# Optimization experiments

Measured on AMD Instinct MI355X. Metric: run time of the kernel, lower is better.

## Reference

```python
import jax, jax.numpy as jnp
import numpy as np


def setup_inputs() -> dict:
    key = jax.random.key(0)
    k1, k2, k3, k4 = jax.random.split(key, 4)
    B, S, d_in, d_out = 4, 2048, 1024, 1024
    x = jax.random.normal(k1, (B, S, d_in), dtype=jnp.float32)
    # weights stored as [d_in, d_out] (transpose of torch Linear weight), scaled like default init
    scale = 1.0 / np.sqrt(d_in)
    Wq = jax.random.normal(k2, (d_in, d_out), dtype=jnp.float32) * scale
    Wk = jax.random.normal(k3, (d_in, d_out), dtype=jnp.float32) * scale
    Wv = jax.random.normal(k4, (d_in, d_out), dtype=jnp.float32) * scale
    return {"x": x, "Wq": Wq, "Wk": Wk, "Wv": Wv}


def reference(x, Wq, Wk, Wv):
    # x: [B, S, d_in]; projections: [B, S, d_out]
    q = jnp.einsum("bsd,de->bse", x, Wq)
    k = jnp.einsum("bsd,de->bse", x, Wk)
    v = jnp.einsum("bsd,de->bse", x, Wv)
    d_out = k.shape[-1]
    # full S x S scores (naive, as in original)
    scores = jnp.einsum("bqe,bke->bqk", q, k)
    # NOTE: original applies softmax over ALL keys first, then multiplies by
    # a lower-triangular causal mask WITHOUT renormalizing. Reproduce exactly.
    weights = jax.nn.softmax(scores / jnp.sqrt(jnp.float32(d_out)), axis=-1)
    S = scores.shape[1]
    mask = jnp.tril(jnp.ones((S, S), dtype=weights.dtype))
    masked = weights * mask  # [B, S, S]
    context = jnp.einsum("bqk,bke->bqe", masked, v)
    return context
```

## Files before the change

kernel.cpp:

```cpp
#include <hip/hip_runtime.h>
#include <hip/hip_bf16.h>
#include <hip/hip_fp16.h>

typedef __attribute__((ext_vector_type(8))) short bf16x8;
typedef __attribute__((ext_vector_type(4))) float f32x4;

__device__ __forceinline__ unsigned short f2bf(float f) {
    unsigned u = __float_as_uint(f);
    u += 0x7fffu + ((u >> 16) & 1u);
    return (unsigned short)(u >> 16);
}

#define GLOAD_LDS16(g, l)                                                           \
    __builtin_amdgcn_global_load_lds(                                               \
        (const __attribute__((address_space(1))) void*)(g),                         \
        (__attribute__((address_space(3))) void*)(l), 16, 0, 0)

#define TBM 256
#define TBN 256
#define TBK 64

template <int OMODE>
__global__ __launch_bounds__(512, 2) void gemm256(
    const unsigned short* __restrict__ A, const unsigned short* __restrict__ B,
    void* __restrict__ Cv, int M, int N, int K,
    long long sA, long long sB, long long sC) {
    __shared__ unsigned short lds[2][4][128 * 64];

    const int bz = blockIdx.z;
    A += (size_t)bz * (size_t)sA;
    B += (size_t)bz * (size_t)sB;

    const int bm = blockIdx.x, bn = blockIdx.y;
    const int tid = threadIdx.x;
    const int wid = tid >> 6, lane = tid & 63;
    const int wr = wid >> 2, wc = wid & 3;
    const int frow = lane & 15, kgrp = lane >> 4;
    const int nt = K / TBK;

    const unsigned short* Abase = A + (size_t)(bm * TBM) * K;
    const unsigned short* Bbase = B + (size_t)(bn * TBN) * K;

    auto STAGE_H = [&](const unsigned short* gtb, int kt, unsigned short* dsthalf) {
#pragma unroll
        for (int ld = 0; ld < 2; ++ld) {
            const int c = tid + ld * 512;
            const int row = c >> 3, c8 = c & 7;
            GLOAD_LDS16(gtb + (size_t)row * K + kt * TBK + ((c8 ^ (row & 7)) << 3),
                        (char*)dsthalf + ld * 8192 + wid * 1024);
        }
    };

    f32x4 acc[8][4];
#pragma unroll
    for (int i = 0; i < 8; ++i)
#pragma unroll
        for (int j = 0; j < 4; ++j) acc[i][j] = (f32x4){0.f, 0.f, 0.f, 0.f};

    STAGE_H(Bbase, 0, &lds[0][2][0]);
    STAGE_H(Bbase + 128 * (size_t)K, 0, &lds[0][3][0]);
    STAGE_H(Abase, 0, &lds[0][0][0]);
    STAGE_H(Abase + 128 * (size_t)K, 0, &lds[0][1][0]);

    for (int t = 0; t < nt; ++t) {
        const int buf = t & 1, bufN = buf ^ 1;
        const unsigned short* Ah = &lds[buf][wr][0];
        const unsigned short* Bh = &lds[buf][2 + (wc >> 1)][0];

        if (t + 1 < nt) {
            STAGE_H(Bbase, t + 1, &lds[bufN][2][0]);
            STAGE_H(Bbase + 128 * (size_t)K, t + 1, &lds[bufN][3][0]);
            asm volatile("s_waitcnt vmcnt(4)" ::: "memory");
        } else {
            asm volatile("s_waitcnt vmcnt(0)" ::: "memory");
        }
        __builtin_amdgcn_s_barrier();

        bf16x8 bfrag[4][2];
#pragma unroll
        for (int n = 0; n < 4; ++n) {
            const int rB = (wc & 1) * 64 + n * 16 + frow;
            const int sw = (rB & 7) << 3;
#pragma unroll
            for (int kk = 0; kk < 2; ++kk)
                bfrag[n][kk] =
                    *(const bf16x8*)&Bh[rB * 64 + ((((kk << 2) + kgrp) << 3) ^ sw)];
        }
        {
            bf16x8 afrag[2][2];
#pragma unroll
            for (int m2 = 0; m2 < 2; ++m2) {
                const int rA = m2 * 16 + frow;
                const int sw = (rA & 7) << 3;
#pragma unroll
                for (int kk = 0; kk < 2; ++kk)
                    afrag[m2][kk] =
                        *(const bf16x8*)&Ah[rA * 64 + ((((kk << 2) + kgrp) << 3) ^ sw)];
            }
            __builtin_amdgcn_s_setprio(1);
#pragma unroll
            for (int m2 = 0; m2 < 2; ++m2)
#pragma unroll
                for (int n = 0; n < 4; ++n)
#pragma unroll
                    for (int kk = 0; kk < 2; ++kk)
                        acc[m2][n] = __builtin_amdgcn_mfma_f32_16x16x32_bf16(
                            afrag[m2][kk], bfrag[n][kk], acc[m2][n], 0, 0, 0);
            __builtin_amdgcn_s_setprio(0);
        }

#pragma unroll
        for (int q = 1; q < 4; ++q) {
            if (q == 1 && t + 1 < nt) STAGE_H(Abase, t + 1, &lds[bufN][0][0]);
            if (q == 2 && t + 1 < nt)
                STAGE_H(Abase + 128 * (size_t)K, t + 1, &lds[bufN][1][0]);
            bf16x8 afrag[2][2];
#pragma unroll
            for (int m2 = 0; m2 < 2; ++m2) {
                const int rA = q * 32 + m2 * 16 + frow;
                const int sw = (rA & 7) << 3;
#pragma unroll
                for (int kk = 0; kk < 2; ++kk)
                    afrag[m2][kk] =
                        *(const bf16x8*)&Ah[rA * 64 + ((((kk << 2) + kgrp) << 3) ^ sw)];
            }
            __builtin_amdgcn_s_setprio(1);
#pragma unroll
            for (int m2 = 0; m2 < 2; ++m2)
#pragma unroll
                for (int n = 0; n < 4; ++n)
#pragma unroll
                    for (int kk = 0; kk < 2; ++kk)
                        acc[q * 2 + m2][n] = __builtin_amdgcn_mfma_f32_16x16x32_bf16(
                            afrag[m2][kk], bfrag[n][kk], acc[q * 2 + m2][n], 0, 0, 0);
            __builtin_amdgcn_s_setprio(0);
        }
    }

    const size_t row0 = (size_t)bm * TBM + wr * 128 + kgrp * 4;
    const int col0 = bn * TBN + wc * 64 + frow;
    if (OMODE == 0) {
        unsigned short* Cp = (unsigned short*)Cv + (size_t)bz * (size_t)sC;
#pragma unroll
        for (int mi = 0; mi < 8; ++mi)
#pragma unroll
            for (int rr = 0; rr < 4; ++rr) {
                unsigned short* op = Cp + (row0 + mi * 16 + rr) * N + col0;
#pragma unroll
                for (int n = 0; n < 4; ++n) op[n * 16] = f2bf(acc[mi][n][rr]);
            }
    } else {
        unsigned short* Cp = (unsigned short*)Cv + (size_t)bz * (size_t)sC;
#pragma unroll
        for (int mi = 0; mi < 8; ++mi)
#pragma unroll
            for (int rr = 0; rr < 4; ++rr) {
                unsigned short* op = Cp + (row0 + mi * 16 + rr) * N + col0;
#pragma unroll
                for (int n = 0; n < 4; ++n)
                    op[n * 16] =
                        __half_as_ushort(__float2half(acc[mi][n][rr] * 0.03125f));
            }
    }
}

#define BM 128
#define BN 128
#define BK 32

__global__ __launch_bounds__(256) void gemm_bt_f32(
    const unsigned short* __restrict__ A, const unsigned short* __restrict__ B,
    float* __restrict__ C, int M, int N, int K,
    long long sA, long long sB, long long sC, int causal) {
    __shared__ unsigned short As[2][BM * BK];
    __shared__ unsigned short Bs[2][BN * BK];

    const int bz = blockIdx.z;
    A += (size_t)bz * (size_t)sA;
    B += (size_t)bz * (size_t)sB;

    const int bm = blockIdx.x, bn = blockIdx.y;
    const int tid = threadIdx.x;
    const int wid = tid >> 6;
    const int lane = tid & 63;
    const int wr = wid >> 1, wc = wid & 1;
    const int frow = lane & 15;
    const int kgrp = lane >> 4;

    int nt = K / BK;
    if (causal) {
        int lim = (bm + 1) * (BM / BK);
        if (lim < nt) nt = lim;
    }

    const int c0 = (wid * 2 + 0) * 64 + lane;
    const int c1 = (wid * 2 + 1) * 64 + lane;
    const unsigned short* Abase = A + (size_t)(bm * BM) * K;
    const unsigned short* Bbase = B + (size_t)(bn * BN) * K;

    auto STAGE = [&](int kt, int buf) {
        const unsigned short* Ag = Abase + kt * BK;
        const unsigned short* Bg = Bbase + kt * BK;
        GLOAD_LDS16(Ag + (size_t)(c0 >> 2) * K + (c0 & 3) * 8,
                    (char*)&As[buf][0] + (wid * 2 + 0) * 1024);
        GLOAD_LDS16(Bg + (size_t)(c0 >> 2) * K + (c0 & 3) * 8,
                    (char*)&Bs[buf][0] + (wid * 2 + 0) * 1024);
        GLOAD_LDS16(Ag + (size_t)(c1 >> 2) * K + (c1 & 3) * 8,
                    (char*)&As[buf][0] + (wid * 2 + 1) * 1024);
        GLOAD_LDS16(Bg + (size_t)(c1 >> 2) * K + (c1 & 3) * 8,
                    (char*)&Bs[buf][0] + (wid * 2 + 1) * 1024);
    };

    f32x4 acc[4][4];
#pragma unroll
    for (int mi = 0; mi < 4; ++mi)
#pragma unroll
        for (int ni = 0; ni < 4; ++ni) acc[mi][ni] = (f32x4){0.f, 0.f, 0.f, 0.f};

    STAGE(0, 0);
    __syncthreads();

    for (int kt = 0; kt < nt; ++kt) {
        const int buf = kt & 1;
        if (kt + 1 < nt) STAGE(kt + 1, buf ^ 1);
        bf16x8 af[4], bfr[4];
#pragma unroll
        for (int mi = 0; mi < 4; ++mi) {
            int row = wr * 64 + mi * 16 + frow;
            af[mi] = *(const bf16x8*)&As[buf][row * BK + kgrp * 8];
        }
#pragma unroll
        for (int ni = 0; ni < 4; ++ni) {
            int col = wc * 64 + ni * 16 + frow;
            bfr[ni] = *(const bf16x8*)&Bs[buf][col * BK + kgrp * 8];
        }
#pragma unroll
        for (int mi = 0; mi < 4; ++mi)
#pragma unroll
            for (int ni = 0; ni < 4; ++ni)
                acc[mi][ni] = __builtin_amdgcn_mfma_f32_16x16x32_bf16(
                    af[mi], bfr[ni], acc[mi][ni], 0, 0, 0);
        __syncthreads();
    }

    const size_t row0 = (size_t)bm * BM + wr * 64 + kgrp * 4;
    const int col0 = bn * BN + wc * 64 + frow;
    float* Cp = C + (size_t)bz * (size_t)sC;
#pragma unroll
    for (int mi = 0; mi < 4; ++mi)
#pragma unroll
        for (int r = 0; r < 4; ++r) {
            float* op = Cp + (row0 + mi * 16 + r) * N + col0;
#pragma unroll
            for (int ni = 0; ni < 4; ++ni) op[ni * 16] = acc[mi][ni][r];
        }
}

__global__ __launch_bounds__(256) void cvt_f32_bf16(
    const float* __restrict__ in, unsigned short* __restrict__ out, int n) {
    int idx = blockIdx.x * blockDim.x + threadIdx.x;
    int stride = gridDim.x * blockDim.x;
    for (int i = idx * 4; i < n; i += stride * 4) {
        float4 v = *(const float4*)(in + i);
        ushort4 o;
        o.x = f2bf(v.x); o.y = f2bf(v.y); o.z = f2bf(v.z); o.w = f2bf(v.w);
        *(ushort4*)(out + i) = o;
    }
}

__global__ __launch_bounds__(256) void transpose_cvt_w(
    const float* __restrict__ in, unsigned short* __restrict__ out, int Kd, int Nd) {
    __shared__ float t[32][33];
    const int bz = blockIdx.z;
    in += (size_t)bz * Kd * Nd;
    out += (size_t)bz * Kd * Nd;
    const int tr = blockIdx.y * 32, tc = blockIdx.x * 32;
    const int r = threadIdx.x >> 3, c4 = (threadIdx.x & 7) * 4;
    float4 v = *(const float4*)&in[(size_t)(tr + r) * Nd + tc + c4];
    t[r][c4 + 0] = v.x; t[r][c4 + 1] = v.y; t[r][c4 + 2] = v.z; t[r][c4 + 3] = v.w;
    __syncthreads();
    ushort4 o;
    o.x = f2bf(t[c4 + 0][r]); o.y = f2bf(t[c4 + 1][r]);
    o.z = f2bf(t[c4 + 2][r]); o.w = f2bf(t[c4 + 3][r]);
    *(ushort4*)&out[(size_t)(tc + r) * Kd + tr + c4] = o;
}

__global__ __launch_bounds__(256) void transpose_bf16(
    const unsigned short* __restrict__ in, unsigned short* __restrict__ out,
    int R, int Cc) {
    __shared__ unsigned short t[32][36];
    const int bz = blockIdx.z;
    in += (size_t)bz * R * Cc;
    out += (size_t)bz * R * Cc;
    const int tr = blockIdx.y * 32, tc = blockIdx.x * 32;
    const int r = threadIdx.x >> 3, c4 = (threadIdx.x & 7) * 4;
    ushort4 v = *(const ushort4*)&in[(size_t)(tr + r) * Cc + tc + c4];
    t[r][c4 + 0] = v.x; t[r][c4 + 1] = v.y; t[r][c4 + 2] = v.z; t[r][c4 + 3] = v.w;
    __syncthreads();
    ushort4 o;
    o.x = t[c4 + 0][r]; o.y = t[c4 + 1][r]; o.z = t[c4 + 2][r]; o.w = t[c4 + 3][r];
    *(ushort4*)&out[(size_t)(tc + r) * R + tr + c4] = o;
}

__global__ __launch_bounds__(256) void softmax_mask(unsigned short* S, int Sd) {
    const int i = blockIdx.x;
    const int b = blockIdx.y;
    unsigned short* row = S + ((size_t)b * Sd + (size_t)i) * Sd;
    const int t = threadIdx.x;
    const int lane = t & 63, wid = t >> 6;

    ushort4 h0 = *(const ushort4*)(row + t * 8);
    ushort4 h1 = *(const ushort4*)(row + t * 8 + 4);
    float v[8];
    v[0] = __half2float(__ushort_as_half(h0.x));
    v[1] = __half2float(__ushort_as_half(h0.y));
    v[2] = __half2float(__ushort_as_half(h0.z));
    v[3] = __half2float(__ushort_as_half(h0.w));
    v[4] = __half2float(__ushort_as_half(h1.x));
    v[5] = __half2float(__ushort_as_half(h1.y));
    v[6] = __half2float(__ushort_as_half(h1.z));
    v[7] = __half2float(__ushort_as_half(h1.w));

    float m = v[0];
#pragma unroll
    for (int j = 1; j < 8; ++j) m = fmaxf(m, v[j]);
#pragma unroll
    for (int o = 32; o; o >>= 1) m = fmaxf(m, __shfl_xor(m, o));
    __shared__ float redm[4];
    __shared__ float reds[4];
    if (lane == 0) redm[wid] = m;
    __syncthreads();
    m = fmaxf(fmaxf(redm[0], redm[1]), fmaxf(redm[2], redm[3]));

    float e[8], s = 0.f;
#pragma unroll
    for (int j = 0; j < 8; ++j) {
        e[j] = __expf(v[j] - m);
        s += e[j];
    }
#pragma unroll
    for (int o = 32; o; o >>= 1) s += __shfl_xor(s, o);
    if (lane == 0) reds[wid] = s;
    __syncthreads();
    s = reds[0] + reds[1] + reds[2] + reds[3];
    const float rinv = 1.0f / s;

    const int base = t * 8;
    ushort4 o0, o1;
    o0.x = (base + 0 <= i) ? f2bf(e[0] * rinv) : 0;
    o0.y = (base + 1 <= i) ? f2bf(e[1] * rinv) : 0;
    o0.z = (base + 2 <= i) ? f2bf(e[2] * rinv) : 0;
    o0.w = (base + 3 <= i) ? f2bf(e[3] * rinv) : 0;
    o1.x = (base + 4 <= i) ? f2bf(e[4] * rinv) : 0;
    o1.y = (base + 5 <= i) ? f2bf(e[5] * rinv) : 0;
    o1.z = (base + 6 <= i) ? f2bf(e[6] * rinv) : 0;
    o1.w = (base + 7 <= i) ? f2bf(e[7] * rinv) : 0;
    *(ushort4*)(row + t * 8) = o0;
    *(ushort4*)(row + t * 8 + 4) = o1;
}

extern "C" void kernel_launch(void* const* d_in, const int* in_sizes, int n_in,
                              void* d_out, int out_size, void* d_ws, size_t ws_size,
                              hipStream_t stream) {
    const int B = 4, S = 2048, D = 1024;
    const size_t M = (size_t)B * S;

    const float* x = (const float*)d_in[0];
    const float* Wq = (const float*)d_in[1];
    float* out = (float*)d_out;

    unsigned short* xb = (unsigned short*)d_ws;
    unsigned short* Wt = xb + M * D;
    unsigned short* Qb = Wt + 3 * (size_t)D * D;
    unsigned short* Kb = Qb + M * D;
    unsigned short* Vb = Kb + M * D;
    unsigned short* Vt = Vb + M * D;
    unsigned short* Sc = Vt + M * D;
    const size_t need =
        (size_t)(M * D * 5 + 3 * (size_t)D * D + (size_t)B * S * S) * 2;
    if (ws_size < need) return;

    cvt_f32_bf16<<<2048, 256, 0, stream>>>(x, xb, (int)(M * D));
    dim3 tg(D / 32, D / 32, 1);
    transpose_cvt_w<<<tg, 256, 0, stream>>>((const float*)d_in[1], Wt + 0 * (size_t)D * D, D, D);
    transpose_cvt_w<<<tg, 256, 0, stream>>>((const float*)d_in[2], Wt + 1 * (size_t)D * D, D, D);
    transpose_cvt_w<<<tg, 256, 0, stream>>>((const float*)d_in[3], Wt + 2 * (size_t)D * D, D, D);
    (void)Wq;

    gemm256<0><<<dim3(M / TBM, D / TBN, 3), 512, 0, stream>>>(
        xb, Wt, (void*)Qb, (int)M, D, D, 0LL, (long long)D * D, (long long)(M * D));

    transpose_bf16<<<dim3(D / 32, S / 32, B), 256, 0, stream>>>(Vb, Vt, S, D);

    gemm256<2><<<dim3(S / TBM, S / TBN, B), 512, 0, stream>>>(
        Qb, Kb, (void*)Sc, S, S, D, (long long)S * D, (long long)S * D,
        (long long)S * S);

    softmax_mask<<<dim3(S, B), 256, 0, stream>>>(Sc, S);

    gemm_bt_f32<<<dim3(S / BM, D / BN, B), 256, 0, stream>>>(
        Sc, Vt, out, S, D, S, (long long)S * S, (long long)D * S,
        (long long)S * D, 1);
}
```

Measured before the change: 181.7 us.

## Restructure gemm256 pipeline with deeper B prefetch, XCD remap, causal reverse order

```diff
diff --git a/kernel.cpp b/kernel.cpp
--- a/kernel.cpp
+++ b/kernel.cpp
@@ -31,7 +31,11 @@
     A += (size_t)bz * (size_t)sA;
     B += (size_t)bz * (size_t)sB;
 
-    const int bm = blockIdx.x, bn = blockIdx.y;
+    const int nwg = gridDim.x * gridDim.y;
+    const int old = blockIdx.y * gridDim.x + blockIdx.x;
+    const int nid = (old & 7) * (nwg >> 3) + (old >> 3);
+    const int bm = nid / gridDim.y, bn = nid % gridDim.y;
+
     const int tid = threadIdx.x;
     const int wid = tid >> 6, lane = tid & 63;
     const int wr = wid >> 2, wc = wid & 3;
@@ -57,63 +61,38 @@
 #pragma unroll
         for (int j = 0; j < 4; ++j) acc[i][j] = (f32x4){0.f, 0.f, 0.f, 0.f};
 
+    STAGE_H(Abase, 0, &lds[0][0][0]);
+    STAGE_H(Abase + 128 * (size_t)K, 0, &lds[0][1][0]);
     STAGE_H(Bbase, 0, &lds[0][2][0]);
     STAGE_H(Bbase + 128 * (size_t)K, 0, &lds[0][3][0]);
-    STAGE_H(Abase, 0, &lds[0][0][0]);
-    STAGE_H(Abase + 128 * (size_t)K, 0, &lds[0][1][0]);
+    if (1 < nt) {
+        STAGE_H(Bbase, 1, &lds[1][2][0]);
+        STAGE_H(Bbase + 128 * (size_t)K, 1, &lds[1][3][0]);
+        asm volatile("s_waitcnt vmcnt(4)" ::: "memory");
+    } else {
+        asm volatile("s_waitcnt vmcnt(0)" ::: "memory");
+    }
+    __builtin_amdgcn_s_barrier();
 
     for (int t = 0; t < nt; ++t) {
-        const int buf = t & 1, bufN = buf ^ 1;
+        const int buf = t & 1;
         const unsigned short* Ah = &lds[buf][wr][0];
         const unsigned short* Bh = &lds[buf][2 + (wc >> 1)][0];
-
-        if (t + 1 < nt) {
-            STAGE_H(Bbase, t + 1, &lds[bufN][2][0]);
-            STAGE_H(Bbase + 128 * (size_t)K, t + 1, &lds[bufN][3][0]);
-            asm volatile("s_waitcnt vmcnt(4)" ::: "memory");
-        } else {
-            asm volatile("s_waitcnt vmcnt(0)" ::: "memory");
-        }
-        __builtin_amdgcn_s_barrier();
-
         bf16x8 bfrag[4][2];
-#pragma unroll
-        for (int n = 0; n < 4; ++n) {
-            const int rB = (wc & 1) * 64 + n * 16 + frow;
-            const int sw = (rB & 7) << 3;
-#pragma unroll
-            for (int kk = 0; kk < 2; ++kk)
-                bfrag[n][kk] =
-                    *(const bf16x8*)&Bh[rB * 64 + ((((kk << 2) + kgrp) << 3) ^ sw)];
-        }
-        {
-            bf16x8 afrag[2][2];
-#pragma unroll
-            for (int m2 = 0; m2 < 2; ++m2) {
-                const int rA = m2 * 16 + frow;
-                const int sw = (rA & 7) << 3;
-#pragma unroll
-                for (int kk = 0; kk < 2; ++kk)
-                    afrag[m2][kk] =
-                        *(const bf16x8*)&Ah[rA * 64 + ((((kk << 2) + kgrp) << 3) ^ sw)];
+
+#pragma unroll
+        for (int q = 0; q < 4; ++q) {
+            if (q == 0) {
+#pragma unroll
+                for (int n = 0; n < 4; ++n) {
+                    const int rB = (wc & 1) * 64 + n * 16 + frow;
+                    const int sw = (rB & 7) << 3;
+#pragma unroll
+                    for (int kk = 0; kk < 2; ++kk)
+                        bfrag[n][kk] = *(const bf16x8*)
+                            &Bh[rB * 64 + ((((kk << 2) + kgrp) << 3) ^ sw)];
+                }
             }
-            __builtin_amdgcn_s_setprio(1);
-#pragma unroll
-            for (int m2 = 0; m2 < 2; ++m2)
-#pragma unroll
-                for (int n = 0; n < 4; ++n)
-#pragma unroll
-                    for (int kk = 0; kk < 2; ++kk)
-                        acc[m2][n] = __builtin_amdgcn_mfma_f32_16x16x32_bf16(
-                            afrag[m2][kk], bfrag[n][kk], acc[m2][n], 0, 0, 0);
-            __builtin_amdgcn_s_setprio(0);
-        }
-
-#pragma unroll
-        for (int q = 1; q < 4; ++q) {
-            if (q == 1 && t + 1 < nt) STAGE_H(Abase, t + 1, &lds[bufN][0][0]);
-            if (q == 2 && t + 1 < nt)
-                STAGE_H(Abase + 128 * (size_t)K, t + 1, &lds[bufN][1][0]);
             bf16x8 afrag[2][2];
 #pragma unroll
             for (int m2 = 0; m2 < 2; ++m2) {
@@ -121,9 +100,21 @@
                 const int sw = (rA & 7) << 3;
 #pragma unroll
                 for (int kk = 0; kk < 2; ++kk)
-                    afrag[m2][kk] =
-                        *(const bf16x8*)&Ah[rA * 64 + ((((kk << 2) + kgrp) << 3) ^ sw)];
+                    afrag[m2][kk] = *(const bf16x8*)
+                        &Ah[rA * 64 + ((((kk << 2) + kgrp) << 3) ^ sw)];
             }
+
+            if (q == 0 && t + 1 < nt) STAGE_H(Abase, t + 1, &lds[buf ^ 1][0][0]);
+            if (q == 1 && t + 1 < nt)
+                STAGE_H(Abase + 128 * (size_t)K, t + 1, &lds[buf ^ 1][1][0]);
+            if (q == 2 && t + 2 < nt) STAGE_H(Bbase, t + 2, &lds[buf][2][0]);
+            if (q == 3 && t + 2 < nt)
+                STAGE_H(Bbase + 128 * (size_t)K, t + 2, &lds[buf][3][0]);
+
+            __builtin_amdgcn_s_barrier();
+            asm volatile("s_waitcnt lgkmcnt(0)" ::: "memory");
+            __builtin_amdgcn_sched_barrier(0);
+
             __builtin_amdgcn_s_setprio(1);
 #pragma unroll
             for (int m2 = 0; m2 < 2; ++m2)
@@ -134,6 +125,15 @@
                         acc[q * 2 + m2][n] = __builtin_amdgcn_mfma_f32_16x16x32_bf16(
                             afrag[m2][kk], bfrag[n][kk], acc[q * 2 + m2][n], 0, 0, 0);
             __builtin_amdgcn_s_setprio(0);
+
+            if (q == 3) {
+                if (t + 2 < nt) {
+                    asm volatile("s_waitcnt vmcnt(4)" ::: "memory");
+                } else {
+                    asm volatile("s_waitcnt vmcnt(0)" ::: "memory");
+                }
+            }
+            __builtin_amdgcn_s_barrier();
         }
     }
 
@@ -179,7 +179,9 @@
     A += (size_t)bz * (size_t)sA;
     B += (size_t)bz * (size_t)sB;
 
-    const int bm = blockIdx.x, bn = blockIdx.y;
+    int bmi = blockIdx.x;
+    if (causal) bmi = gridDim.x - 1 - bmi;
+    const int bm = bmi, bn = blockIdx.y;
     const int tid = threadIdx.x;
     const int wid = tid >> 6;
     const int lane = tid & 63;
@@ -271,9 +273,6 @@
 __global__ __launch_bounds__(256) void transpose_cvt_w(
     const float* __restrict__ in, unsigned short* __restrict__ out, int Kd, int Nd) {
     __shared__ float t[32][33];
-    const int bz = blockIdx.z;
-    in += (size_t)bz * Kd * Nd;
-    out += (size_t)bz * Kd * Nd;
     const int tr = blockIdx.y * 32, tc = blockIdx.x * 32;
     const int r = threadIdx.x >> 3, c4 = (threadIdx.x & 7) * 4;
     float4 v = *(const float4*)&in[(size_t)(tr + r) * Nd + tc + c4];
@@ -366,7 +365,6 @@
     const size_t M = (size_t)B * S;
 
     const float* x = (const float*)d_in[0];
-    const float* Wq = (const float*)d_in[1];
     float* out = (float*)d_out;
 
     unsigned short* xb = (unsigned short*)d_ws;
@@ -385,7 +383,6 @@
     transpose_cvt_w<<<tg, 256, 0, stream>>>((const float*)d_in[1], Wt + 0 * (size_t)D * D, D, D);
     transpose_cvt_w<<<tg, 256, 0, stream>>>((const float*)d_in[2], Wt + 1 * (size_t)D * D, D, D);
     transpose_cvt_w<<<tg, 256, 0, stream>>>((const float*)d_in[3], Wt + 2 * (size_t)D * D, D, D);
-    (void)Wq;
 
     gemm256<0><<<dim3(M / TBM, D / TBN, 3), 512, 0, stream>>>(
         xb, Wt, (void*)Qb, (int)M, D, D, 0LL, (long long)D * D, (long long)(M * D));
```

Measured after the change: 190.2 us. 1.05x slower.

## Fuse softmax into QK epilogue row sums and PV operand load

Applied to the files above, without the earlier changes.

```diff
diff --git a/kernel.cpp b/kernel.cpp
--- a/kernel.cpp
+++ b/kernel.cpp
@@ -3,6 +3,7 @@
 #include <hip/hip_fp16.h>
 
 typedef __attribute__((ext_vector_type(8))) short bf16x8;
+typedef __attribute__((ext_vector_type(8))) unsigned short u16x8;
 typedef __attribute__((ext_vector_type(4))) float f32x4;
 
 __device__ __forceinline__ unsigned short f2bf(float f) {
@@ -23,7 +24,7 @@
 template <int OMODE>
 __global__ __launch_bounds__(512, 2) void gemm256(
     const unsigned short* __restrict__ A, const unsigned short* __restrict__ B,
-    void* __restrict__ Cv, int M, int N, int K,
+    void* __restrict__ Cv, float* __restrict__ Zb, int M, int N, int K,
     long long sA, long long sB, long long sC) {
     __shared__ unsigned short lds[2][4][128 * 64];
 
@@ -151,65 +152,106 @@
             }
     } else {
         unsigned short* Cp = (unsigned short*)Cv + (size_t)bz * (size_t)sC;
+        float rs[8][4];
 #pragma unroll
         for (int mi = 0; mi < 8; ++mi)
 #pragma unroll
             for (int rr = 0; rr < 4; ++rr) {
                 unsigned short* op = Cp + (row0 + mi * 16 + rr) * N + col0;
-#pragma unroll
-                for (int n = 0; n < 4; ++n)
-                    op[n * 16] =
-                        __half_as_ushort(__float2half(acc[mi][n][rr] * 0.03125f));
-            }
+                float p = 0.f;
+#pragma unroll
+                for (int n = 0; n < 4; ++n) {
+                    __half h = __float2half(acc[mi][n][rr] * 0.03125f);
+                    op[n * 16] = __half_as_ushort(h);
+                    p += __expf(__half2float(h));
+                }
+                rs[mi][rr] = p;
+            }
+#pragma unroll
+        for (int mi = 0; mi < 8; ++mi)
+#pragma unroll
+            for (int rr = 0; rr < 4; ++rr) {
+                float v = rs[mi][rr];
+                v += __shfl_xor(v, 1);
+                v += __shfl_xor(v, 2);
+                v += __shfl_xor(v, 4);
+                v += __shfl_xor(v, 8);
+                rs[mi][rr] = v;
+            }
+        if (frow == 0) {
+            float* Zr = Zb + (size_t)bz * M + row0;
+#pragma unroll
+            for (int mi = 0; mi < 8; ++mi)
+#pragma unroll
+                for (int rr = 0; rr < 4; ++rr)
+                    atomicAdd(&Zr[mi * 16 + rr], rs[mi][rr]);
+        }
     }
 }
 
-#define BM 128
-#define BN 128
-#define BK 32
-
-__global__ __launch_bounds__(256) void gemm_bt_f32(
-    const unsigned short* __restrict__ A, const unsigned short* __restrict__ B,
-    float* __restrict__ C, int M, int N, int K,
-    long long sA, long long sB, long long sC, int causal) {
-    __shared__ unsigned short As[2][BM * BK];
-    __shared__ unsigned short Bs[2][BN * BK];
+#define PBM 128
+#define PBN 128
+#define PBK 32
+
+__global__ __launch_bounds__(256) void pv_fused(
+    const unsigned short* __restrict__ Sh, const unsigned short* __restrict__ Vt,
+    float* __restrict__ C, const float* __restrict__ Z, int Sd, int Dd) {
+    __shared__ unsigned short As[2][PBM * PBK];
+    __shared__ unsigned short Bs[2][PBN * PBK];
+    __shared__ float rinv_s[PBM];
 
     const int bz = blockIdx.z;
-    A += (size_t)bz * (size_t)sA;
-    B += (size_t)bz * (size_t)sB;
-
-    const int bm = blockIdx.x, bn = blockIdx.y;
+    const int bm = gridDim.x - 1 - blockIdx.x;
+    const int bn = blockIdx.y;
     const int tid = threadIdx.x;
-    const int wid = tid >> 6;
-    const int lane = tid & 63;
+    const int wid = tid >> 6, lane = tid & 63;
     const int wr = wid >> 1, wc = wid & 1;
-    const int frow = lane & 15;
-    const int kgrp = lane >> 4;
-
-    int nt = K / BK;
-    if (causal) {
-        int lim = (bm + 1) * (BM / BK);
-        if (lim < nt) nt = lim;
-    }
-
-    const int c0 = (wid * 2 + 0) * 64 + lane;
-    const int c1 = (wid * 2 + 1) * 64 + lane;
-    const unsigned short* Abase = A + (size_t)(bm * BM) * K;
-    const unsigned short* Bbase = B + (size_t)(bn * BN) * K;
-
-    auto STAGE = [&](int kt, int buf) {
-        const unsigned short* Ag = Abase + kt * BK;
-        const unsigned short* Bg = Bbase + kt * BK;
-        GLOAD_LDS16(Ag + (size_t)(c0 >> 2) * K + (c0 & 3) * 8,
-                    (char*)&As[buf][0] + (wid * 2 + 0) * 1024);
-        GLOAD_LDS16(Bg + (size_t)(c0 >> 2) * K + (c0 & 3) * 8,
-                    (char*)&Bs[buf][0] + (wid * 2 + 0) * 1024);
-        GLOAD_LDS16(Ag + (size_t)(c1 >> 2) * K + (c1 & 3) * 8,
-                    (char*)&As[buf][0] + (wid * 2 + 1) * 1024);
-        GLOAD_LDS16(Bg + (size_t)(c1 >> 2) * K + (c1 & 3) * 8,
-                    (char*)&Bs[buf][0] + (wid * 2 + 1) * 1024);
+    const int frow = lane & 15, kgrp = lane >> 4;
+
+    const unsigned short* Sb =
+        Sh + (size_t)bz * Sd * Sd + (size_t)(bm * PBM) * Sd;
+    const unsigned short* Vb =
+        Vt + (size_t)bz * (size_t)Dd * Sd + (size_t)(bn * PBN) * Sd;
+
+    const int nt = (bm + 1) * (PBM / PBK);
+
+    if (tid < PBM) rinv_s[tid] = 1.0f / Z[(size_t)bz * Sd + bm * PBM + tid];
+
+    auto LOAD_A = [&](int kt, u16x8* areg) {
+#pragma unroll
+        for (int ld = 0; ld < 2; ++ld) {
+            const int c = tid + ld * 256;
+            areg[ld] = *(const u16x8*)(Sb + (size_t)(c >> 2) * Sd + kt * PBK +
+                                       (c & 3) * 8);
+        }
     };
+    auto STAGE_B = [&](int kt, int buf) {
+#pragma unroll
+        for (int ld = 0; ld < 2; ++ld) {
+            const int c = tid + ld * 256;
+            GLOAD_LDS16(Vb + (size_t)(c >> 2) * Sd + kt * PBK + (c & 3) * 8,
+                        (char*)&Bs[buf][0] + (wid * 64 + ld * 256) * 16);
+        }
+    };
+    auto XFORM_WRITE = [&](int kt, int buf, const u16x8* areg) {
+#pragma unroll
+        for (int ld = 0; ld < 2; ++ld) {
+            const int c = tid + ld * 256;
+            const int row = c >> 2;
+            const int rowg = bm * PBM + row;
+            const int colg0 = kt * PBK + (c & 3) * 8;
+            const float ri = rinv_s[row];
+            bf16x8 o;
+#pragma unroll
+            for (int j = 0; j < 8; ++j) {
+                float e = __expf(__half2float(__ushort_as_half(
+                              (unsigned short)areg[ld][j]))) *
+                          ri;
+                o[j] = (colg0 + j <= rowg) ? (short)f2bf(e) : (short)0;
+            }
+            *(bf16x8*)((char*)&As[buf][0] + c * 16) = o;
+        }
+    };
 
     f32x4 acc[4][4];
 #pragma unroll
@@ -217,22 +259,30 @@
 #pragma unroll
         for (int ni = 0; ni < 4; ++ni) acc[mi][ni] = (f32x4){0.f, 0.f, 0.f, 0.f};
 
-    STAGE(0, 0);
+    u16x8 areg[2];
+    LOAD_A(0, areg);
+    STAGE_B(0, 0);
     __syncthreads();
-
-    for (int kt = 0; kt < nt; ++kt) {
-        const int buf = kt & 1;
-        if (kt + 1 < nt) STAGE(kt + 1, buf ^ 1);
+    XFORM_WRITE(0, 0, areg);
+    __syncthreads();
+
+    for (int t = 0; t < nt; ++t) {
+        const int buf = t & 1;
+        u16x8 anext[2];
+        if (t + 1 < nt) {
+            LOAD_A(t + 1, anext);
+            STAGE_B(t + 1, buf ^ 1);
+        }
         bf16x8 af[4], bfr[4];
 #pragma unroll
         for (int mi = 0; mi < 4; ++mi) {
             int row = wr * 64 + mi * 16 + frow;
-            af[mi] = *(const bf16x8*)&As[buf][row * BK + kgrp * 8];
+            af[mi] = *(const bf16x8*)&As[buf][row * PBK + kgrp * 8];
         }
 #pragma unroll
         for (int ni = 0; ni < 4; ++ni) {
             int col = wc * 64 + ni * 16 + frow;
-            bfr[ni] = *(const bf16x8*)&Bs[buf][col * BK + kgrp * 8];
+            bfr[ni] = *(const bf16x8*)&Bs[buf][col * PBK + kgrp * 8];
         }
 #pragma unroll
         for (int mi = 0; mi < 4; ++mi)
@@ -240,20 +290,26 @@
             for (int ni = 0; ni < 4; ++ni)
                 acc[mi][ni] = __builtin_amdgcn_mfma_f32_16x16x32_bf16(
                     af[mi], bfr[ni], acc[mi][ni], 0, 0, 0);
+        if (t + 1 < nt) XFORM_WRITE(t + 1, buf ^ 1, anext);
         __syncthreads();
     }
 
-    const size_t row0 = (size_t)bm * BM + wr * 64 + kgrp * 4;
-    const int col0 = bn * BN + wc * 64 + frow;
-    float* Cp = C + (size_t)bz * (size_t)sC;
+    const size_t row0 = (size_t)bm * PBM + wr * 64 + kgrp * 4;
+    const int col0 = bn * PBN + wc * 64 + frow;
+    float* Cp = C + (size_t)bz * (size_t)Sd * Dd;
 #pragma unroll
     for (int mi = 0; mi < 4; ++mi)
 #pragma unroll
         for (int r = 0; r < 4; ++r) {
-            float* op = Cp + (row0 + mi * 16 + r) * N + col0;
+            float* op = Cp + (row0 + mi * 16 + r) * Dd + col0;
 #pragma unroll
             for (int ni = 0; ni < 4; ++ni) op[ni * 16] = acc[mi][ni][r];
         }
+}
+
+__global__ __launch_bounds__(256) void zero_f32(float* __restrict__ p, int n) {
+    int i = blockIdx.x * blockDim.x + threadIdx.x;
+    if (i < n) p[i] = 0.f;
 }
 
 __global__ __launch_bounds__(256) void cvt_f32_bf16(
@@ -271,9 +327,6 @@
 __global__ __launch_bounds__(256) void transpose_cvt_w(
     const float* __restrict__ in, unsigned short* __restrict__ out, int Kd, int Nd) {
     __shared__ float t[32][33];
-    const int bz = blockIdx.z;
-    in += (size_t)bz * Kd * Nd;
-    out += (size_t)bz * Kd * Nd;
     const int tr = blockIdx.y * 32, tc = blockIdx.x * 32;
     const int r = threadIdx.x >> 3, c4 = (threadIdx.x & 7) * 4;
     float4 v = *(const float4*)&in[(size_t)(tr + r) * Nd + tc + c4];
@@ -302,63 +355,6 @@
     *(ushort4*)&out[(size_t)(tc + r) * R + tr + c4] = o;
 }
 
-__global__ __launch_bounds__(256) void softmax_mask(unsigned short* S, int Sd) {
-    const int i = blockIdx.x;
-    const int b = blockIdx.y;
-    unsigned short* row = S + ((size_t)b * Sd + (size_t)i) * Sd;
-    const int t = threadIdx.x;
-    const int lane = t & 63, wid = t >> 6;
-
-    ushort4 h0 = *(const ushort4*)(row + t * 8);
-    ushort4 h1 = *(const ushort4*)(row + t * 8 + 4);
-    float v[8];
-    v[0] = __half2float(__ushort_as_half(h0.x));
-    v[1] = __half2float(__ushort_as_half(h0.y));
-    v[2] = __half2float(__ushort_as_half(h0.z));
-    v[3] = __half2float(__ushort_as_half(h0.w));
-    v[4] = __half2float(__ushort_as_half(h1.x));
-    v[5] = __half2float(__ushort_as_half(h1.y));
-    v[6] = __half2float(__ushort_as_half(h1.z));
-    v[7] = __half2float(__ushort_as_half(h1.w));
-
-    float m = v[0];
-#pragma unroll
-    for (int j = 1; j < 8; ++j) m = fmaxf(m, v[j]);
-#pragma unroll
-    for (int o = 32; o; o >>= 1) m = fmaxf(m, __shfl_xor(m, o));
-    __shared__ float redm[4];
-    __shared__ float reds[4];
-    if (lane == 0) redm[wid] = m;
-    __syncthreads();
-    m = fmaxf(fmaxf(redm[0], redm[1]), fmaxf(redm[2], redm[3]));
-
-    float e[8], s = 0.f;
-#pragma unroll
-    for (int j = 0; j < 8; ++j) {
-        e[j] = __expf(v[j] - m);
-        s += e[j];
-    }
-#pragma unroll
-    for (int o = 32; o; o >>= 1) s += __shfl_xor(s, o);
-    if (lane == 0) reds[wid] = s;
-    __syncthreads();
-    s = reds[0] + reds[1] + reds[2] + reds[3];
-    const float rinv = 1.0f / s;
-
-    const int base = t * 8;
-    ushort4 o0, o1;
-    o0.x = (base + 0 <= i) ? f2bf(e[0] * rinv) : 0;
-    o0.y = (base + 1 <= i) ? f2bf(e[1] * rinv) : 0;
-    o0.z = (base + 2 <= i) ? f2bf(e[2] * rinv) : 0;
-    o0.w = (base + 3 <= i) ? f2bf(e[3] * rinv) : 0;
-    o1.x = (base + 4 <= i) ? f2bf(e[4] * rinv) : 0;
-    o1.y = (base + 5 <= i) ? f2bf(e[5] * rinv) : 0;
-    o1.z = (base + 6 <= i) ? f2bf(e[6] * rinv) : 0;
-    o1.w = (base + 7 <= i) ? f2bf(e[7] * rinv) : 0;
-    *(ushort4*)(row + t * 8) = o0;
-    *(ushort4*)(row + t * 8 + 4) = o1;
-}
-
 extern "C" void kernel_launch(void* const* d_in, const int* in_sizes, int n_in,
                               void* d_out, int out_size, void* d_ws, size_t ws_size,
                               hipStream_t stream) {
@@ -366,7 +362,6 @@
     const size_t M = (size_t)B * S;
 
     const float* x = (const float*)d_in[0];
-    const float* Wq = (const float*)d_in[1];
     float* out = (float*)d_out;
 
     unsigned short* xb = (unsigned short*)d_ws;
@@ -376,29 +371,29 @@
     unsigned short* Vb = Kb + M * D;
     unsigned short* Vt = Vb + M * D;
     unsigned short* Sc = Vt + M * D;
+    float* Zd = (float*)(Sc + (size_t)B * S * S);
     const size_t need =
-        (size_t)(M * D * 5 + 3 * (size_t)D * D + (size_t)B * S * S) * 2;
+        (size_t)(M * D * 5 + 3 * (size_t)D * D + (size_t)B * S * S) * 2 +
+        (size_t)B * S * 4;
     if (ws_size < need) return;
 
+    zero_f32<<<(B * S + 255) / 256, 256, 0, stream>>>(Zd, B * S);
     cvt_f32_bf16<<<2048, 256, 0, stream>>>(x, xb, (int)(M * D));
     dim3 tg(D / 32, D / 32, 1);
     transpose_cvt_w<<<tg, 256, 0, stream>>>((const float*)d_in[1], Wt + 0 * (size_t)D * D, D, D);
     transpose_cvt_w<<<tg, 256, 0, stream>>>((const float*)d_in[2], Wt + 1 * (size_t)D * D, D, D);
     transpose_cvt_w<<<tg, 256, 0, stream>>>((const float*)d_in[3], Wt + 2 * (size_t)D * D, D, D);
-    (void)Wq;
 
     gemm256<0><<<dim3(M / TBM, D / TBN, 3), 512, 0, stream>>>(
-        xb, Wt, (void*)Qb, (int)M, D, D, 0LL, (long long)D * D, (long long)(M * D));
+        xb, Wt, (void*)Qb, nullptr, (int)M, D, D, 0LL, (long long)D * D,
+        (long long)(M * D));
 
     transpose_bf16<<<dim3(D / 32, S / 32, B), 256, 0, stream>>>(Vb, Vt, S, D);
 
     gemm256<2><<<dim3(S / TBM, S / TBN, B), 512, 0, stream>>>(
-        Qb, Kb, (void*)Sc, S, S, D, (long long)S * D, (long long)S * D,
+        Qb, Kb, (void*)Sc, Zd, S, S, D, (long long)S * D, (long long)S * D,
         (long long)S * S);
 
-    softmax_mask<<<dim3(S, B), 256, 0, stream>>>(Sc, S);
-
-    gemm_bt_f32<<<dim3(S / BM, D / BN, B), 256, 0, stream>>>(
-        Sc, Vt, out, S, D, S, (long long)S * S, (long long)D * S,
-        (long long)S * D, 1);
-}
+    pv_fused<<<dim3(S / PBM, D / PBN, B), 256, 0, stream>>>(
+        Sc, Vt, out, Zd, S, D);
+}
```

New measurement: 219.1 us. 20.6% more time.

## Fuse softmax exp and row sums into QK^T epilogue, normalize in PV

Applied to the files above, without the earlier changes.

```diff
diff --git a/kernel.cpp b/kernel.cpp
--- a/kernel.cpp
+++ b/kernel.cpp
@@ -10,6 +10,9 @@
     u += 0x7fffu + ((u >> 16) & 1u);
     return (unsigned short)(u >> 16);
 }
+__device__ __forceinline__ float bf2f(unsigned short b) {
+    return __uint_as_float(((unsigned)b) << 16);
+}
 
 #define GLOAD_LDS16(g, l)                                                           \
     __builtin_amdgcn_global_load_lds(                                               \
@@ -23,7 +26,7 @@
 template <int OMODE>
 __global__ __launch_bounds__(512, 2) void gemm256(
     const unsigned short* __restrict__ A, const unsigned short* __restrict__ B,
-    void* __restrict__ Cv, int M, int N, int K,
+    void* __restrict__ Cv, float* __restrict__ Zb, int M, int N, int K,
     long long sA, long long sB, long long sC) {
     __shared__ unsigned short lds[2][4][128 * 64];
 
@@ -151,16 +154,42 @@
             }
     } else {
         unsigned short* Cp = (unsigned short*)Cv + (size_t)bz * (size_t)sC;
+        float rs[8][4];
 #pragma unroll
         for (int mi = 0; mi < 8; ++mi)
 #pragma unroll
             for (int rr = 0; rr < 4; ++rr) {
-                unsigned short* op = Cp + (row0 + mi * 16 + rr) * N + col0;
-#pragma unroll
-                for (int n = 0; n < 4; ++n)
-                    op[n * 16] =
-                        __half_as_ushort(__float2half(acc[mi][n][rr] * 0.03125f));
-            }
+                const int rowg = (int)(row0 + mi * 16 + rr);
+                unsigned short* op = Cp + (size_t)rowg * N + col0;
+                float zsum = 0.f;
+#pragma unroll
+                for (int n = 0; n < 4; ++n) {
+                    float e = __expf(acc[mi][n][rr] * 0.03125f);
+                    unsigned short pb = f2bf(e);
+                    zsum += bf2f(pb);
+                    op[n * 16] = (col0 + n * 16 <= rowg) ? pb : (unsigned short)0;
+                }
+                rs[mi][rr] = zsum;
+            }
+#pragma unroll
+        for (int mi = 0; mi < 8; ++mi)
+#pragma unroll
+            for (int rr = 0; rr < 4; ++rr) {
+                float v = rs[mi][rr];
+                v += __shfl_xor(v, 1);
+                v += __shfl_xor(v, 2);
+                v += __shfl_xor(v, 4);
+                v += __shfl_xor(v, 8);
+                rs[mi][rr] = v;
+            }
+        if (frow == 0) {
+            float* Zr = Zb + (size_t)bz * M + row0;
+#pragma unroll
+            for (int mi = 0; mi < 8; ++mi)
+#pragma unroll
+                for (int rr = 0; rr < 4; ++rr)
+                    atomicAdd(&Zr[mi * 16 + rr], rs[mi][rr]);
+        }
     }
 }
 
@@ -168,10 +197,10 @@
 #define BN 128
 #define BK 32
 
-__global__ __launch_bounds__(256) void gemm_bt_f32(
+__global__ __launch_bounds__(256) void gemm_pv(
     const unsigned short* __restrict__ A, const unsigned short* __restrict__ B,
-    float* __restrict__ C, int M, int N, int K,
-    long long sA, long long sB, long long sC, int causal) {
+    float* __restrict__ C, const float* __restrict__ Z, int M, int N, int K,
+    long long sA, long long sB, long long sC) {
     __shared__ unsigned short As[2][BM * BK];
     __shared__ unsigned short Bs[2][BN * BK];
 
@@ -179,7 +208,8 @@
     A += (size_t)bz * (size_t)sA;
     B += (size_t)bz * (size_t)sB;
 
-    const int bm = blockIdx.x, bn = blockIdx.y;
+    const int bm = gridDim.x - 1 - blockIdx.x;
+    const int bn = blockIdx.y;
     const int tid = threadIdx.x;
     const int wid = tid >> 6;
     const int lane = tid & 63;
@@ -188,7 +218,7 @@
     const int kgrp = lane >> 4;
 
     int nt = K / BK;
-    if (causal) {
+    {
         int lim = (bm + 1) * (BM / BK);
         if (lim < nt) nt = lim;
     }
@@ -246,14 +276,21 @@
     const size_t row0 = (size_t)bm * BM + wr * 64 + kgrp * 4;
     const int col0 = bn * BN + wc * 64 + frow;
     float* Cp = C + (size_t)bz * (size_t)sC;
+    const float* Zp = Z + (size_t)bz * M;
 #pragma unroll
     for (int mi = 0; mi < 4; ++mi)
 #pragma unroll
         for (int r = 0; r < 4; ++r) {
+            const float ri = 1.0f / Zp[row0 + mi * 16 + r];
             float* op = Cp + (row0 + mi * 16 + r) * N + col0;
 #pragma unroll
-            for (int ni = 0; ni < 4; ++ni) op[ni * 16] = acc[mi][ni][r];
-        }
+            for (int ni = 0; ni < 4; ++ni) op[ni * 16] = acc[mi][ni][r] * ri;
+        }
+}
+
+__global__ __launch_bounds__(256) void zero_f32(float* __restrict__ p, int n) {
+    int i = blockIdx.x * blockDim.x + threadIdx.x;
+    if (i < n) p[i] = 0.f;
 }
 
 __global__ __launch_bounds__(256) void cvt_f32_bf16(
@@ -271,9 +308,6 @@
 __global__ __launch_bounds__(256) void transpose_cvt_w(
     const float* __restrict__ in, unsigned short* __restrict__ out, int Kd, int Nd) {
     __shared__ float t[32][33];
-    const int bz = blockIdx.z;
-    in += (size_t)bz * Kd * Nd;
-    out += (size_t)bz * Kd * Nd;
     const int tr = blockIdx.y * 32, tc = blockIdx.x * 32;
     const int r = threadIdx.x >> 3, c4 = (threadIdx.x & 7) * 4;
     float4 v = *(const float4*)&in[(size_t)(tr + r) * Nd + tc + c4];
@@ -302,63 +336,6 @@
     *(ushort4*)&out[(size_t)(tc + r) * R + tr + c4] = o;
 }
 
-__global__ __launch_bounds__(256) void softmax_mask(unsigned short* S, int Sd) {
-    const int i = blockIdx.x;
-    const int b = blockIdx.y;
-    unsigned short* row = S + ((size_t)b * Sd + (size_t)i) * Sd;
-    const int t = threadIdx.x;
-    const int lane = t & 63, wid = t >> 6;
-
-    ushort4 h0 = *(const ushort4*)(row + t * 8);
-    ushort4 h1 = *(const ushort4*)(row + t * 8 + 4);
-    float v[8];
-    v[0] = __half2float(__ushort_as_half(h0.x));
-    v[1] = __half2float(__ushort_as_half(h0.y));
-    v[2] = __half2float(__ushort_as_half(h0.z));
-    v[3] = __half2float(__ushort_as_half(h0.w));
-    v[4] = __half2float(__ushort_as_half(h1.x));
-    v[5] = __half2float(__ushort_as_half(h1.y));
-    v[6] = __half2float(__ushort_as_half(h1.z));
-    v[7] = __half2float(__ushort_as_half(h1.w));
-
-    float m = v[0];
-#pragma unroll
-    for (int j = 1; j < 8; ++j) m = fmaxf(m, v[j]);
-#pragma unroll
-    for (int o = 32; o; o >>= 1) m = fmaxf(m, __shfl_xor(m, o));
-    __shared__ float redm[4];
-    __shared__ float reds[4];
-    if (lane == 0) redm[wid] = m;
-    __syncthreads();
-    m = fmaxf(fmaxf(redm[0], redm[1]), fmaxf(redm[2], redm[3]));
-
-    float e[8], s = 0.f;
-#pragma unroll
-    for (int j = 0; j < 8; ++j) {
-        e[j] = __expf(v[j] - m);
-        s += e[j];
-    }
-#pragma unroll
-    for (int o = 32; o; o >>= 1) s += __shfl_xor(s, o);
-    if (lane == 0) reds[wid] = s;
-    __syncthreads();
-    s = reds[0] + reds[1] + reds[2] + reds[3];
-    const float rinv = 1.0f / s;
-
-    const int base = t * 8;
-    ushort4 o0, o1;
-    o0.x = (base + 0 <= i) ? f2bf(e[0] * rinv) : 0;
-    o0.y = (base + 1 <= i) ? f2bf(e[1] * rinv) : 0;
-    o0.z = (base + 2 <= i) ? f2bf(e[2] * rinv) : 0;
-    o0.w = (base + 3 <= i) ? f2bf(e[3] * rinv) : 0;
-    o1.x = (base + 4 <= i) ? f2bf(e[4] * rinv) : 0;
-    o1.y = (base + 5 <= i) ? f2bf(e[5] * rinv) : 0;
-    o1.z = (base + 6 <= i) ? f2bf(e[6] * rinv) : 0;
-    o1.w = (base + 7 <= i) ? f2bf(e[7] * rinv) : 0;
-    *(ushort4*)(row + t * 8) = o0;
-    *(ushort4*)(row + t * 8 + 4) = o1;
-}
-
 extern "C" void kernel_launch(void* const* d_in, const int* in_sizes, int n_in,
                               void* d_out, int out_size, void* d_ws, size_t ws_size,
                               hipStream_t stream) {
@@ -366,7 +343,6 @@
     const size_t M = (size_t)B * S;
 
     const float* x = (const float*)d_in[0];
-    const float* Wq = (const float*)d_in[1];
     float* out = (float*)d_out;
 
     unsigned short* xb = (unsigned short*)d_ws;
@@ -376,29 +352,30 @@
     unsigned short* Vb = Kb + M * D;
     unsigned short* Vt = Vb + M * D;
     unsigned short* Sc = Vt + M * D;
+    float* Zd = (float*)(Sc + (size_t)B * S * S);
     const size_t need =
-        (size_t)(M * D * 5 + 3 * (size_t)D * D + (size_t)B * S * S) * 2;
+        (size_t)(M * D * 5 + 3 * (size_t)D * D + (size_t)B * S * S) * 2 +
+        (size_t)B * S * 4;
     if (ws_size < need) return;
 
+    zero_f32<<<(B * S + 255) / 256, 256, 0, stream>>>(Zd, B * S);
     cvt_f32_bf16<<<2048, 256, 0, stream>>>(x, xb, (int)(M * D));
     dim3 tg(D / 32, D / 32, 1);
     transpose_cvt_w<<<tg, 256, 0, stream>>>((const float*)d_in[1], Wt + 0 * (size_t)D * D, D, D);
     transpose_cvt_w<<<tg, 256, 0, stream>>>((const float*)d_in[2], Wt + 1 * (size_t)D * D, D, D);
     transpose_cvt_w<<<tg, 256, 0, stream>>>((const float*)d_in[3], Wt + 2 * (size_t)D * D, D, D);
-    (void)Wq;
 
     gemm256<0><<<dim3(M / TBM, D / TBN, 3), 512, 0, stream>>>(
-        xb, Wt, (void*)Qb, (int)M, D, D, 0LL, (long long)D * D, (long long)(M * D));
+        xb, Wt, (void*)Qb, nullptr, (int)M, D, D, 0LL, (long long)D * D,
+        (long long)(M * D));
 
     transpose_bf16<<<dim3(D / 32, S / 32, B), 256, 0, stream>>>(Vb, Vt, S, D);
 
     gemm256<2><<<dim3(S / TBM, S / TBN, B), 512, 0, stream>>>(
-        Qb, Kb, (void*)Sc, S, S, D, (long long)S * D, (long long)S * D,
+        Qb, Kb, (void*)Sc, Zd, S, S, D, (long long)S * D, (long long)S * D,
         (long long)S * S);
 
-    softmax_mask<<<dim3(S, B), 256, 0, stream>>>(Sc, S);
-
-    gemm_bt_f32<<<dim3(S / BM, D / BN, B), 256, 0, stream>>>(
-        Sc, Vt, out, S, D, S, (long long)S * S, (long long)D * S,
-        (long long)S * D, 1);
-}
+    gemm_pv<<<dim3(S / BM, D / BN, B), 256, 0, stream>>>(
+        Sc, Vt, out, Zd, S, D, S, (long long)S * S, (long long)D * S,
+        (long long)S * D);
+}
```

After: 180.5 us. No clear change (-0.7%).
